# Performance work log

Hardware: AMD Instinct MI355X
Metric: run time of the kernel (lower is better)

The kernel has to match this reference:

```python
import jax, jax.numpy as jnp
import numpy as np

N_HEADS = 16
D_HEAD = 64  # embed_dim // n_heads = 1024 // 16


def setup_inputs() -> dict:
    key = jax.random.key(0)
    ks = jax.random.split(key, 8)
    B, S, E = 2, 2048, 1024
    return {
        "k_in": jax.random.normal(ks[0], (B, S, E), jnp.float32),
        "q_in": jax.random.normal(ks[1], (B, S, E), jnp.float32),
        "v_in": jax.random.normal(ks[2], (B, S, E), jnp.float32),
        "Wq": jax.random.normal(ks[3], (D_HEAD, D_HEAD), jnp.float32) / np.sqrt(D_HEAD),
        "Wk": jax.random.normal(ks[4], (D_HEAD, D_HEAD), jnp.float32) / np.sqrt(D_HEAD),
        "Wv": jax.random.normal(ks[5], (D_HEAD, D_HEAD), jnp.float32) / np.sqrt(D_HEAD),
        "Wo": jax.random.normal(ks[6], (E, E), jnp.float32) / np.sqrt(E),
        "bo": jnp.zeros((E,), jnp.float32),
    }


def reference(k_in, q_in, v_in, Wq, Wk, Wv, Wo, bo):
    B, Sq, E = q_in.shape
    Sk = k_in.shape[1]
    H, Dh = N_HEADS, D_HEAD
    # split heads: [B, S, H, Dh]
    q = q_in.reshape(B, Sq, H, Dh)
    k = k_in.reshape(B, Sk, H, Dh)
    v = v_in.reshape(B, Sk, H, Dh)
    # per-head linear projections (nn.Linear: x @ W.T), then [B, H, S, Dh]
    q = jnp.einsum("bshd,ed->bhse", q, Wq)
    k = jnp.einsum("bshd,ed->bhse", k, Wk)
    v = jnp.einsum("bshd,ed->bhse", v, Wv)
    # scaled dot-product attention
    scores = jnp.einsum("bhqd,bhkd->bhqk", q, k) / jnp.sqrt(jnp.asarray(Dh, q.dtype))
    attn = jax.nn.softmax(scores, axis=-1)
    ctx = jnp.einsum("bhqk,bhkd->bqhd", attn, v)  # [B, Sq, H, Dh]
    concat = ctx.reshape(B, Sq, H * Dh)
    return concat @ Wo.T + bo
```

## Files before the change

### kernel.cpp

```cpp
#include <hip/hip_runtime.h>
#include <hip/hip_fp16.h>

typedef _Float16 f16;
typedef _Float16 f16x8 __attribute__((ext_vector_type(8)));
typedef _Float16 f16x4v __attribute__((ext_vector_type(4)));
typedef float f32x4 __attribute__((ext_vector_type(4)));

#define B_ 2
#define S_ 2048
#define E_ 1024
#define H_ 16
#define DH_ 64

__device__ __forceinline__ f32x4 mfma16(f16x8 a, f16x8 b, f32x4 c) {
    return __builtin_amdgcn_mfma_f32_16x16x32_f16(a, b, c, 0, 0, 0);
}

__device__ __forceinline__ f32x4 vmax4(f32x4 a, f32x4 b) {
    f32x4 r;
    r[0] = fmaxf(a[0], b[0]); r[1] = fmaxf(a[1], b[1]);
    r[2] = fmaxf(a[2], b[2]); r[3] = fmaxf(a[3], b[3]);
    return r;
}

__device__ __forceinline__ f16x8 cvt8(const float* p) {
    float4 v0 = *(const float4*)p;
    float4 v1 = *(const float4*)(p + 4);
    f16x8 r;
    r[0] = (f16)v0.x; r[1] = (f16)v0.y; r[2] = (f16)v0.z; r[3] = (f16)v0.w;
    r[4] = (f16)v1.x; r[5] = (f16)v1.y; r[6] = (f16)v1.z; r[7] = (f16)v1.w;
    return r;
}

__global__ __launch_bounds__(256) void proj_kernel(
    const float* __restrict__ q_in, const float* __restrict__ k_in,
    const float* __restrict__ v_in,
    const float* __restrict__ Wq, const float* __restrict__ Wk,
    const float* __restrict__ Wv,
    f16* __restrict__ Qg, f16* __restrict__ Kg, f16* __restrict__ Vt)
{
    int tid = threadIdx.x;
    int lane = tid & 63, wv = tid >> 6;
    int wid = blockIdx.x * 4 + wv;
    int proj = wid >> 12;
    int r = wid & 4095;
    int bh = r >> 7;
    int stile = r & 127;
    int sbase = stile * 16;
    int h = bh & 15;
    int b = bh >> 4;
    int c = lane & 15, g = lane >> 4;

    const float* x; const float* W;
    if (proj == 0)      { x = q_in; W = Wq; }
    else if (proj == 1) { x = k_in; W = Wk; }
    else                { x = v_in; W = Wv; }

    const float* xrow = x + (((size_t)(b * S_ + sbase + c) * H_ + h) << 6);
    f16x8 a0 = cvt8(xrow + g * 8);
    f16x8 a1 = cvt8(xrow + 32 + g * 8);

    f32x4 acc[4] = {};
#pragma unroll
    for (int nt = 0; nt < 4; ++nt) {
        const float* wrow = W + ((nt * 16 + c) << 6);
        f16x8 b0 = cvt8(wrow + g * 8);
        f16x8 b1 = cvt8(wrow + 32 + g * 8);
        acc[nt] = mfma16(a0, b0, acc[nt]);
        acc[nt] = mfma16(a1, b1, acc[nt]);
    }

    if (proj < 2) {
        f16* out = (proj == 0) ? Qg : Kg;
#pragma unroll
        for (int nt = 0; nt < 4; ++nt)
#pragma unroll
            for (int j = 0; j < 4; ++j) {
                int s = sbase + g * 4 + j;
                out[((size_t)bh * S_ + s) * DH_ + nt * 16 + c] = (f16)acc[nt][j];
            }
    } else {
#pragma unroll
        for (int nt = 0; nt < 4; ++nt) {
            f16x4v pk;
            pk[0] = (f16)acc[nt][0]; pk[1] = (f16)acc[nt][1];
            pk[2] = (f16)acc[nt][2]; pk[3] = (f16)acc[nt][3];
            *(f16x4v*)&Vt[((size_t)bh * DH_ + nt * 16 + c) * S_ + sbase + g * 4] = pk;
        }
    }
}

__global__ __launch_bounds__(256) void cvt_wo(const float* __restrict__ W,
                                              f16* __restrict__ out)
{
    int i = blockIdx.x * 256 + threadIdx.x;
    float4 v = *(const float4*)(W + (size_t)i * 4);
    f16x4v o;
    o[0] = (f16)v.x; o[1] = (f16)v.y; o[2] = (f16)v.z; o[3] = (f16)v.w;
    *(f16x4v*)(out + (size_t)i * 4) = o;
}

#define C1_ 0.18033688011112042f

__global__ __launch_bounds__(512, 4) void attn_kernel(
    const f16* __restrict__ Qg, const f16* __restrict__ Kg,
    const f16* __restrict__ Vt, f16* __restrict__ ctx)
{
    __shared__ __align__(16) f16 Kl[2][128 * 64];
    __shared__ __align__(16) f16 Vl[2][2][64 * 64];
    __shared__ __align__(16) f16 Pl[8][16 * 64];

    int tid = threadIdx.x, lane = tid & 63, wv = tid >> 6;
    int bid = blockIdx.x;
    int sb = (bid & 7) * 64 + (bid >> 3);
    int bh = sb >> 4, qt = sb & 15;
    int b = bh >> 4, h = bh & 15;
    int qbase = qt * 128 + wv * 16;
    int c = lane & 15, g = lane >> 4;
    int swz = (c & 7) << 3;

    const f16* Qh = Qg + (size_t)bh * S_ * DH_;
    const f16* Kh = Kg + (size_t)bh * S_ * DH_;
    const f16* Vh = Vt + (size_t)bh * DH_ * S_;

    int s0 = tid, s1 = tid + 512;
    int kr0 = s0 >> 3, kc0 = s0 & 7, kr1 = s1 >> 3, kc1 = s1 & 7;
    int kd0 = kr0 * 64 + ((kc0 * 8) ^ ((kr0 & 7) << 3));
    int kd1 = kr1 * 64 + ((kc1 * 8) ^ ((kr1 & 7) << 3));
    const f16* ksp0 = Kh + kr0 * 64 + kc0 * 8;
    const f16* ksp1 = Kh + kr1 * 64 + kc1 * 8;
    int vr0 = s0 >> 4, vc0 = s0 & 15, vr1 = s1 >> 4, vc1 = s1 & 15;
    int vst0 = vc0 >> 3, vst1 = vc1 >> 3;
    int vd0 = vr0 * 64 + (((vc0 & 7) * 8) ^ ((vr0 & 7) << 3));
    int vd1 = vr1 * 64 + (((vc1 & 7) * 8) ^ ((vr1 & 7) << 3));
    const f16* vsp0 = Vh + vr0 * S_ + vc0 * 8;
    const f16* vsp1 = Vh + vr1 * S_ + vc1 * 8;

    f16x8 qf[2];
#pragma unroll
    for (int hh = 0; hh < 2; ++hh)
        qf[hh] = *(const f16x8*)(Qh + (size_t)(qbase + c) * DH_ + hh * 32 + g * 8);

    float m2 = -1e30f;
    f32x4 lrv = {};
    f32x4 accO[4] = {};
    f16x8 kreg0, kreg1, vreg0, vreg1;

    kreg0 = *(const f16x8*)ksp0; kreg1 = *(const f16x8*)ksp1;
    vreg0 = *(const f16x8*)vsp0; vreg1 = *(const f16x8*)vsp1;
    *(f16x8*)&Kl[0][kd0] = kreg0; *(f16x8*)&Kl[0][kd1] = kreg1;
    *(f16x8*)&Vl[0][vst0][vd0] = vreg0; *(f16x8*)&Vl[0][vst1][vd1] = vreg1;
    __syncthreads();

#define ATTN_STEP(CUR, T, STAGE)                                               \
    do {                                                                       \
        if (STAGE) {                                                           \
            int ko = ((T) + 1) * 128 * 64, vo = ((T) + 1) * 128;               \
            kreg0 = *(const f16x8*)(ksp0 + ko);                                \
            kreg1 = *(const f16x8*)(ksp1 + ko);                                \
            vreg0 = *(const f16x8*)(vsp0 + vo);                                \
            vreg1 = *(const f16x8*)(vsp1 + vo);                                \
        }                                                                      \
        _Pragma("unroll")                                                      \
        for (int st = 0; st < 2; ++st) {                                       \
            f32x4 accS[4] = {};                                                \
            __builtin_amdgcn_s_setprio(1);                                     \
            _Pragma("unroll")                                                  \
            for (int ks = 0; ks < 4; ++ks) {                                   \
                int krow = (st * 64 + ks * 16 + c) * 64;                       \
                f16x8 k0 = *(const f16x8*)&Kl[CUR][krow + ((8 * g) ^ swz)];    \
                f16x8 k1 = *(const f16x8*)&Kl[CUR][krow + ((32 + 8 * g) ^ swz)];\
                accS[ks] = mfma16(k0, qf[0], accS[ks]);                        \
                accS[ks] = mfma16(k1, qf[1], accS[ks]);                        \
            }                                                                  \
            __builtin_amdgcn_s_setprio(0);                                     \
            f32x4 mx4 = vmax4(vmax4(accS[0], accS[1]), vmax4(accS[2], accS[3]));\
            float rmax = fmaxf(fmaxf(mx4[0], mx4[1]), fmaxf(mx4[2], mx4[3]));  \
            if (!__all(fmaf(rmax, C1_, -m2) <= 8.f)) {                         \
                float mx = fmaxf(rmax, __shfl_xor(rmax, 16));                  \
                mx = fmaxf(mx, __shfl_xor(mx, 32));                            \
                float mn = fmaxf(m2, mx * C1_);                                \
                float al = exp2f(m2 - mn);                                     \
                m2 = mn;                                                       \
                _Pragma("unroll")                                              \
                for (int j = 0; j < 4; ++j) lrv[j] *= al;                      \
                _Pragma("unroll")                                              \
                for (int j = 0; j < 4; ++j) {                                  \
                    float aj = __shfl(al, 4 * g + j);                          \
                    _Pragma("unroll")                                          \
                    for (int nt = 0; nt < 4; ++nt) accO[nt][j] *= aj;          \
                }                                                              \
            }                                                                  \
            _Pragma("unroll")                                                  \
            for (int ks = 0; ks < 4; ++ks) {                                   \
                f32x4 e;                                                       \
                _Pragma("unroll")                                              \
                for (int j = 0; j < 4; ++j)                                    \
                    e[j] = exp2f(fmaf(accS[ks][j], C1_, -m2));                 \
                lrv += e;                                                      \
                f16x4v w;                                                      \
                w[0] = (f16)e[0]; w[1] = (f16)e[1];                            \
                w[2] = (f16)e[2]; w[3] = (f16)e[3];                            \
                *(f16x4v*)&Pl[wv][c * 64 + ((16 * ks + 4 * g) ^ swz)] = w;     \
            }                                                                  \
            __builtin_amdgcn_s_setprio(1);                                     \
            _Pragma("unroll")                                                  \
            for (int kh = 0; kh < 2; ++kh) {                                   \
                f16x8 pa = *(const f16x8*)&Pl[wv][c * 64                       \
                                + (((st * 64 + 32 * kh + 8 * g) & 63) ^ swz)]; \
                _Pragma("unroll")                                              \
                for (int nt = 0; nt < 4; ++nt) {                               \
                    f16x8 vb = *(const f16x8*)&Vl[CUR][st][(nt * 16 + c) * 64  \
                                    + ((32 * kh + 8 * g) ^ swz)];              \
                    accO[nt] = mfma16(pa, vb, accO[nt]);                       \
                }                                                              \
            }                                                                  \
            __builtin_amdgcn_s_setprio(0);                                     \
        }                                                                      \
        if (STAGE) {                                                           \
            int nb = (CUR) ^ 1;                                                \
            *(f16x8*)&Kl[nb][kd0] = kreg0; *(f16x8*)&Kl[nb][kd1] = kreg1;      \
            *(f16x8*)&Vl[nb][vst0][vd0] = vreg0;                               \
            *(f16x8*)&Vl[nb][vst1][vd1] = vreg1;                               \
            __syncthreads();                                                   \
        }                                                                      \
    } while (0)

#pragma unroll 1
    for (int kt = 0; kt < 14; kt += 2) {
        ATTN_STEP(0, kt, 1);
        ATTN_STEP(1, kt + 1, 1);
    }
    ATTN_STEP(0, 14, 1);
    ATTN_STEP(1, 15, 0);
#undef ATTN_STEP

    float lr = (lrv[0] + lrv[1]) + (lrv[2] + lrv[3]);
    lr += __shfl_xor(lr, 16);
    lr += __shfl_xor(lr, 32);
    float inv = 1.f / lr;
#pragma unroll
    for (int j = 0; j < 4; ++j) {
        float lj = __shfl(inv, 4 * g + j);
        int s = qbase + 4 * g + j;
#pragma unroll
        for (int nt = 0; nt < 4; ++nt)
            ctx[((size_t)b * S_ + s) * E_ + h * DH_ + nt * 16 + c] =
                (f16)(accO[nt][j] * lj);
    }
}

__global__ __launch_bounds__(256) void gemm_out(
    const f16* __restrict__ A,
    const f16* __restrict__ Bw,
    const float* __restrict__ bo,
    float* __restrict__ out)
{
    __shared__ __align__(16) f16 Al[2][128 * 64];
    __shared__ __align__(16) f16 Bl[2][64 * 64];

    int tid = threadIdx.x, lane = tid & 63, wv = tid >> 6;
    int bid = blockIdx.x;
    int sb = (bid & 7) * 64 + (bid >> 3);
    int mbase = (sb & 31) * 128, nbase = (sb >> 5) * 64;
    int c = lane & 15, g = lane >> 4;
    int wr = wv >> 1, wc = wv & 1;
    int swz = (c & 7) << 3;

    int adst[4]; const f16* asrc[4];
#pragma unroll
    for (int i = 0; i < 4; ++i) {
        int slot = tid + i * 256;
        int row = slot >> 3, cc = slot & 7;
        adst[i] = row * 64 + ((cc * 8) ^ ((row & 7) << 3));
        asrc[i] = A + (size_t)(mbase + row) * 1024 + cc * 8;
    }
    int bdst[2]; const f16* bsrc[2];
#pragma unroll
    for (int i = 0; i < 2; ++i) {
        int slot = tid + i * 256;
        int row = slot >> 3, cc = slot & 7;
        bdst[i] = row * 64 + ((cc * 8) ^ ((row & 7) << 3));
        bsrc[i] = Bw + (size_t)(nbase + row) * 1024 + cc * 8;
    }

    f32x4 acc[4][2] = {};
    f16x8 areg[4], breg[2];

#pragma unroll
    for (int i = 0; i < 4; ++i) areg[i] = *(const f16x8*)asrc[i];
#pragma unroll
    for (int i = 0; i < 2; ++i) breg[i] = *(const f16x8*)bsrc[i];
#pragma unroll
    for (int i = 0; i < 4; ++i) *(f16x8*)&Al[0][adst[i]] = areg[i];
#pragma unroll
    for (int i = 0; i < 2; ++i) *(f16x8*)&Bl[0][bdst[i]] = breg[i];
    __syncthreads();

#define GEMM_STEP(CUR, T, STAGE)                                               \
    do {                                                                       \
        if (STAGE) {                                                           \
            _Pragma("unroll")                                                  \
            for (int i = 0; i < 4; ++i)                                        \
                areg[i] = *(const f16x8*)(asrc[i] + ((T) + 1) * 64);           \
            _Pragma("unroll")                                                  \
            for (int i = 0; i < 2; ++i)                                        \
                breg[i] = *(const f16x8*)(bsrc[i] + ((T) + 1) * 64);           \
        }                                                                      \
        __builtin_amdgcn_s_setprio(1);                                         \
        _Pragma("unroll")                                                      \
        for (int kk = 0; kk < 2; ++kk) {                                       \
            f16x8 af[4], bf[2];                                                \
            _Pragma("unroll")                                                  \
            for (int mi = 0; mi < 4; ++mi)                                     \
                af[mi] = *(const f16x8*)&Al[CUR][(wr * 64 + mi * 16 + c) * 64  \
                                               + ((32 * kk + 8 * g) ^ swz)];   \
            _Pragma("unroll")                                                  \
            for (int ni = 0; ni < 2; ++ni)                                     \
                bf[ni] = *(const f16x8*)&Bl[CUR][(wc * 32 + ni * 16 + c) * 64  \
                                               + ((32 * kk + 8 * g) ^ swz)];   \
            _Pragma("unroll")                                                  \
            for (int mi = 0; mi < 4; ++mi)                                     \
                _Pragma("unroll")                                              \
                for (int ni = 0; ni < 2; ++ni)                                 \
                    acc[mi][ni] = mfma16(af[mi], bf[ni], acc[mi][ni]);         \
        }                                                                      \
        __builtin_amdgcn_s_setprio(0);                                         \
        if (STAGE) {                                                           \
            int nb = (CUR) ^ 1;                                                \
            _Pragma("unroll")                                                  \
            for (int i = 0; i < 4; ++i) *(f16x8*)&Al[nb][adst[i]] = areg[i];   \
            _Pragma("unroll")                                                  \
            for (int i = 0; i < 2; ++i) *(f16x8*)&Bl[nb][bdst[i]] = breg[i];   \
            __syncthreads();                                                   \
        }                                                                      \
    } while (0)

#pragma unroll 1
    for (int ks = 0; ks < 14; ks += 2) {
        GEMM_STEP(0, ks, 1);
        GEMM_STEP(1, ks + 1, 1);
    }
    GEMM_STEP(0, 14, 1);
    GEMM_STEP(1, 15, 0);
#undef GEMM_STEP

#pragma unroll
    for (int ni = 0; ni < 2; ++ni) {
        float bias = bo[nbase + wc * 32 + ni * 16 + c];
#pragma unroll
        for (int mi = 0; mi < 4; ++mi)
#pragma unroll
            for (int j = 0; j < 4; ++j) {
                int m = mbase + wr * 64 + mi * 16 + g * 4 + j;
                out[(size_t)m * 1024 + nbase + wc * 32 + ni * 16 + c] =
                    acc[mi][ni][j] + bias;
            }
    }
}

extern "C" void kernel_launch(void* const* d_in, const int* in_sizes, int n_in,
                              void* d_out, int out_size, void* d_ws, size_t ws_size,
                              hipStream_t stream)
{
    const float* k_in = (const float*)d_in[0];
    const float* q_in = (const float*)d_in[1];
    const float* v_in = (const float*)d_in[2];
    const float* Wq   = (const float*)d_in[3];
    const float* Wk   = (const float*)d_in[4];
    const float* Wv   = (const float*)d_in[5];
    const float* Wo   = (const float*)d_in[6];
    const float* bo   = (const float*)d_in[7];
    float* out = (float*)d_out;

    char* ws = (char*)d_ws;
    f16* Qg  = (f16*)(ws);
    f16* Kg  = (f16*)(ws + (8u << 20));
    f16* Vt  = (f16*)(ws + (16u << 20));
    f16* ctx = (f16*)(ws + (24u << 20));
    f16* WoH = (f16*)(ws + (32u << 20));

    proj_kernel<<<dim3(3072), dim3(256), 0, stream>>>(q_in, k_in, v_in,
                                                      Wq, Wk, Wv, Qg, Kg, Vt);
    cvt_wo<<<dim3(1024), dim3(256), 0, stream>>>(Wo, WoH);
    attn_kernel<<<dim3(512), dim3(512), 0, stream>>>(Qg, Kg, Vt, ctx);
    gemm_out<<<dim3(512), dim3(256), 0, stream>>>(ctx, WoH, bo, out);
}
```

Before: 115.0 us.

## Shrink attention tiles to 64 keys and 256 threads, fuse Wo conversion into projection

```diff
diff --git a/kernel.cpp b/kernel.cpp
--- a/kernel.cpp
+++ b/kernel.cpp
@@ -2,6 +2,7 @@
 #include <hip/hip_fp16.h>
 
 typedef _Float16 f16;
+typedef __fp16 hf16x2 __attribute__((ext_vector_type(2)));
 typedef _Float16 f16x8 __attribute__((ext_vector_type(8)));
 typedef _Float16 f16x4v __attribute__((ext_vector_type(4)));
 typedef float f32x4 __attribute__((ext_vector_type(4)));
@@ -32,16 +33,27 @@
     return r;
 }
 
-__global__ __launch_bounds__(256) void proj_kernel(
+__global__ __launch_bounds__(256) void proj_cvt_kernel(
     const float* __restrict__ q_in, const float* __restrict__ k_in,
     const float* __restrict__ v_in,
     const float* __restrict__ Wq, const float* __restrict__ Wk,
-    const float* __restrict__ Wv,
-    f16* __restrict__ Qg, f16* __restrict__ Kg, f16* __restrict__ Vt)
+    const float* __restrict__ Wv, const float* __restrict__ Wo,
+    f16* __restrict__ Qg, f16* __restrict__ Kg, f16* __restrict__ Vt,
+    f16* __restrict__ WoH)
 {
     int tid = threadIdx.x;
+    int bx = blockIdx.x;
+    if (bx >= 3072) {
+        int i = (bx - 3072) * 256 + tid;
+        float4 v = *(const float4*)(Wo + (size_t)i * 4);
+        f16x4v o;
+        o[0] = (f16)v.x; o[1] = (f16)v.y; o[2] = (f16)v.z; o[3] = (f16)v.w;
+        *(f16x4v*)(WoH + (size_t)i * 4) = o;
+        return;
+    }
+
     int lane = tid & 63, wv = tid >> 6;
-    int wid = blockIdx.x * 4 + wv;
+    int wid = bx * 4 + wv;
     int proj = wid >> 12;
     int r = wid & 4095;
     int bh = r >> 7;
@@ -90,32 +102,22 @@
     }
 }
 
-__global__ __launch_bounds__(256) void cvt_wo(const float* __restrict__ W,
-                                              f16* __restrict__ out)
-{
-    int i = blockIdx.x * 256 + threadIdx.x;
-    float4 v = *(const float4*)(W + (size_t)i * 4);
-    f16x4v o;
-    o[0] = (f16)v.x; o[1] = (f16)v.y; o[2] = (f16)v.z; o[3] = (f16)v.w;
-    *(f16x4v*)(out + (size_t)i * 4) = o;
-}
-
 #define C1_ 0.18033688011112042f
 
-__global__ __launch_bounds__(512, 4) void attn_kernel(
+__global__ __launch_bounds__(256, 4) void attn_kernel(
     const f16* __restrict__ Qg, const f16* __restrict__ Kg,
     const f16* __restrict__ Vt, f16* __restrict__ ctx)
 {
-    __shared__ __align__(16) f16 Kl[2][128 * 64];
-    __shared__ __align__(16) f16 Vl[2][2][64 * 64];
-    __shared__ __align__(16) f16 Pl[8][16 * 64];
+    __shared__ __align__(16) f16 Kl[2][64 * 64];
+    __shared__ __align__(16) f16 Vl[2][64 * 64];
+    __shared__ __align__(16) f16 Pl[4][16 * 64];
 
     int tid = threadIdx.x, lane = tid & 63, wv = tid >> 6;
     int bid = blockIdx.x;
-    int sb = (bid & 7) * 64 + (bid >> 3);
-    int bh = sb >> 4, qt = sb & 15;
+    int sb = (bid & 7) * 128 + (bid >> 3);
+    int bh = sb >> 5, qt = sb & 31;
     int b = bh >> 4, h = bh & 15;
-    int qbase = qt * 128 + wv * 16;
+    int qbase = qt * 64 + wv * 16;
     int c = lane & 15, g = lane >> 4;
     int swz = (c & 7) << 3;
 
@@ -123,18 +125,14 @@
     const f16* Kh = Kg + (size_t)bh * S_ * DH_;
     const f16* Vh = Vt + (size_t)bh * DH_ * S_;
 
-    int s0 = tid, s1 = tid + 512;
+    int s0 = tid, s1 = tid + 256;
     int kr0 = s0 >> 3, kc0 = s0 & 7, kr1 = s1 >> 3, kc1 = s1 & 7;
     int kd0 = kr0 * 64 + ((kc0 * 8) ^ ((kr0 & 7) << 3));
     int kd1 = kr1 * 64 + ((kc1 * 8) ^ ((kr1 & 7) << 3));
     const f16* ksp0 = Kh + kr0 * 64 + kc0 * 8;
     const f16* ksp1 = Kh + kr1 * 64 + kc1 * 8;
-    int vr0 = s0 >> 4, vc0 = s0 & 15, vr1 = s1 >> 4, vc1 = s1 & 15;
-    int vst0 = vc0 >> 3, vst1 = vc1 >> 3;
-    int vd0 = vr0 * 64 + (((vc0 & 7) * 8) ^ ((vr0 & 7) << 3));
-    int vd1 = vr1 * 64 + (((vc1 & 7) * 8) ^ ((vr1 & 7) << 3));
-    const f16* vsp0 = Vh + vr0 * S_ + vc0 * 8;
-    const f16* vsp1 = Vh + vr1 * S_ + vc1 * 8;
+    const f16* vsp0 = Vh + kr0 * S_ + kc0 * 8;
+    const f16* vsp1 = Vh + kr1 * S_ + kc1 * 8;
 
     f16x8 qf[2];
 #pragma unroll
@@ -149,90 +147,87 @@
     kreg0 = *(const f16x8*)ksp0; kreg1 = *(const f16x8*)ksp1;
     vreg0 = *(const f16x8*)vsp0; vreg1 = *(const f16x8*)vsp1;
     *(f16x8*)&Kl[0][kd0] = kreg0; *(f16x8*)&Kl[0][kd1] = kreg1;
-    *(f16x8*)&Vl[0][vst0][vd0] = vreg0; *(f16x8*)&Vl[0][vst1][vd1] = vreg1;
+    *(f16x8*)&Vl[0][kd0] = vreg0; *(f16x8*)&Vl[0][kd1] = vreg1;
     __syncthreads();
 
 #define ATTN_STEP(CUR, T, STAGE)                                               \
     do {                                                                       \
         if (STAGE) {                                                           \
-            int ko = ((T) + 1) * 128 * 64, vo = ((T) + 1) * 128;               \
+            int ko = ((T) + 1) * 64 * 64, vo = ((T) + 1) * 64;                 \
             kreg0 = *(const f16x8*)(ksp0 + ko);                                \
             kreg1 = *(const f16x8*)(ksp1 + ko);                                \
             vreg0 = *(const f16x8*)(vsp0 + vo);                                \
             vreg1 = *(const f16x8*)(vsp1 + vo);                                \
         }                                                                      \
+        f32x4 accS[4] = {};                                                    \
+        __builtin_amdgcn_s_setprio(1);                                         \
         _Pragma("unroll")                                                      \
-        for (int st = 0; st < 2; ++st) {                                       \
-            f32x4 accS[4] = {};                                                \
-            __builtin_amdgcn_s_setprio(1);                                     \
-            _Pragma("unroll")                                                  \
-            for (int ks = 0; ks < 4; ++ks) {                                   \
-                int krow = (st * 64 + ks * 16 + c) * 64;                       \
-                f16x8 k0 = *(const f16x8*)&Kl[CUR][krow + ((8 * g) ^ swz)];    \
-                f16x8 k1 = *(const f16x8*)&Kl[CUR][krow + ((32 + 8 * g) ^ swz)];\
-                accS[ks] = mfma16(k0, qf[0], accS[ks]);                        \
-                accS[ks] = mfma16(k1, qf[1], accS[ks]);                        \
+        for (int ks = 0; ks < 4; ++ks) {                                       \
+            int krow = (ks * 16 + c) * 64;                                     \
+            f16x8 k0 = *(const f16x8*)&Kl[CUR][krow + ((8 * g) ^ swz)];        \
+            f16x8 k1 = *(const f16x8*)&Kl[CUR][krow + ((32 + 8 * g) ^ swz)];   \
+            accS[ks] = mfma16(k0, qf[0], accS[ks]);                            \
+            accS[ks] = mfma16(k1, qf[1], accS[ks]);                            \
+        }                                                                      \
+        __builtin_amdgcn_s_setprio(0);                                         \
+        f32x4 mx4 = vmax4(vmax4(accS[0], accS[1]), vmax4(accS[2], accS[3]));   \
+        float rmax = fmaxf(fmaxf(mx4[0], mx4[1]), fmaxf(mx4[2], mx4[3]));      \
+        if (!__all(fmaf(rmax, C1_, -m2) <= 8.f)) {                             \
+            float mx = fmaxf(rmax, __shfl_xor(rmax, 16));                      \
+            mx = fmaxf(mx, __shfl_xor(mx, 32));                                \
+            float mn = fmaxf(m2, mx * C1_);                                    \
+            float al = exp2f(m2 - mn);                                         \
+            m2 = mn;                                                           \
+            _Pragma("unroll")                                                  \
+            for (int j = 0; j < 4; ++j) lrv[j] *= al;                          \
+            _Pragma("unroll")                                                  \
+            for (int j = 0; j < 4; ++j) {                                      \
+                float aj = __shfl(al, 4 * g + j);                              \
+                _Pragma("unroll")                                              \
+                for (int nt = 0; nt < 4; ++nt) accO[nt][j] *= aj;              \
             }                                                                  \
-            __builtin_amdgcn_s_setprio(0);                                     \
-            f32x4 mx4 = vmax4(vmax4(accS[0], accS[1]), vmax4(accS[2], accS[3]));\
-            float rmax = fmaxf(fmaxf(mx4[0], mx4[1]), fmaxf(mx4[2], mx4[3]));  \
-            if (!__all(fmaf(rmax, C1_, -m2) <= 8.f)) {                         \
-                float mx = fmaxf(rmax, __shfl_xor(rmax, 16));                  \
-                mx = fmaxf(mx, __shfl_xor(mx, 32));                            \
-                float mn = fmaxf(m2, mx * C1_);                                \
-                float al = exp2f(m2 - mn);                                     \
-                m2 = mn;                                                       \
-                _Pragma("unroll")                                              \
-                for (int j = 0; j < 4; ++j) lrv[j] *= al;                      \
-                _Pragma("unroll")                                              \
-                for (int j = 0; j < 4; ++j) {                                  \
-                    float aj = __shfl(al, 4 * g + j);                          \
-                    _Pragma("unroll")                                          \
-                    for (int nt = 0; nt < 4; ++nt) accO[nt][j] *= aj;          \
-                }                                                              \
+        }                                                                      \
+        _Pragma("unroll")                                                      \
+        for (int ks = 0; ks < 4; ++ks) {                                       \
+            f32x4 e;                                                           \
+            _Pragma("unroll")                                                  \
+            for (int j = 0; j < 4; ++j)                                        \
+                e[j] = exp2f(fmaf(accS[ks][j], C1_, -m2));                     \
+            lrv += e;                                                          \
+            hf16x2 lo = __builtin_amdgcn_cvt_pkrtz(e[0], e[1]);                \
+            hf16x2 hi = __builtin_amdgcn_cvt_pkrtz(e[2], e[3]);                \
+            uint2 w;                                                           \
+            w.x = __builtin_bit_cast(unsigned, lo);                            \
+            w.y = __builtin_bit_cast(unsigned, hi);                            \
+            *(uint2*)&Pl[wv][c * 64 + ((16 * ks + 4 * g) ^ swz)] = w;          \
+        }                                                                      \
+        __builtin_amdgcn_s_setprio(1);                                         \
+        _Pragma("unroll")                                                      \
+        for (int kh = 0; kh < 2; ++kh) {                                       \
+            f16x8 pa = *(const f16x8*)&Pl[wv][c * 64 + ((32 * kh + 8 * g) ^ swz)];\
+            _Pragma("unroll")                                                  \
+            for (int nt = 0; nt < 4; ++nt) {                                   \
+                f16x8 vb = *(const f16x8*)&Vl[CUR][(nt * 16 + c) * 64          \
+                                + ((32 * kh + 8 * g) ^ swz)];                  \
+                accO[nt] = mfma16(pa, vb, accO[nt]);                           \
             }                                                                  \
-            _Pragma("unroll")                                                  \
-            for (int ks = 0; ks < 4; ++ks) {                                   \
-                f32x4 e;                                                       \
-                _Pragma("unroll")                                              \
-                for (int j = 0; j < 4; ++j)                                    \
-                    e[j] = exp2f(fmaf(accS[ks][j], C1_, -m2));                 \
-                lrv += e;                                                      \
-                f16x4v w;                                                      \
-                w[0] = (f16)e[0]; w[1] = (f16)e[1];                            \
-                w[2] = (f16)e[2]; w[3] = (f16)e[3];                            \
-                *(f16x4v*)&Pl[wv][c * 64 + ((16 * ks + 4 * g) ^ swz)] = w;     \
-            }                                                                  \
-            __builtin_amdgcn_s_setprio(1);                                     \
-            _Pragma("unroll")                                                  \
-            for (int kh = 0; kh < 2; ++kh) {                                   \
-                f16x8 pa = *(const f16x8*)&Pl[wv][c * 64                       \
-                                + (((st * 64 + 32 * kh + 8 * g) & 63) ^ swz)]; \
-                _Pragma("unroll")                                              \
-                for (int nt = 0; nt < 4; ++nt) {                               \
-                    f16x8 vb = *(const f16x8*)&Vl[CUR][st][(nt * 16 + c) * 64  \
-                                    + ((32 * kh + 8 * g) ^ swz)];              \
-                    accO[nt] = mfma16(pa, vb, accO[nt]);                       \
-                }                                                              \
-            }                                                                  \
-            __builtin_amdgcn_s_setprio(0);                                     \
-        }                                                                      \
+        }                                                                      \
+        __builtin_amdgcn_s_setprio(0);                                         \
         if (STAGE) {                                                           \
             int nb = (CUR) ^ 1;                                                \
             *(f16x8*)&Kl[nb][kd0] = kreg0; *(f16x8*)&Kl[nb][kd1] = kreg1;      \
-            *(f16x8*)&Vl[nb][vst0][vd0] = vreg0;                               \
-            *(f16x8*)&Vl[nb][vst1][vd1] = vreg1;                               \
+            *(f16x8*)&Vl[nb][kd0] = vreg0; *(f16x8*)&Vl[nb][kd1] = vreg1;      \
             __syncthreads();                                                   \
         }                                                                      \
     } while (0)
 
 #pragma unroll 1
-    for (int kt = 0; kt < 14; kt += 2) {
+    for (int kt = 0; kt < 30; kt += 2) {
         ATTN_STEP(0, kt, 1);
         ATTN_STEP(1, kt + 1, 1);
     }
-    ATTN_STEP(0, 14, 1);
-    ATTN_STEP(1, 15, 0);
+    ATTN_STEP(0, 30, 1);
+    ATTN_STEP(1, 31, 0);
 #undef ATTN_STEP
 
     float lr = (lrv[0] + lrv[1]) + (lrv[2] + lrv[3]);
@@ -380,9 +375,8 @@
     f16* ctx = (f16*)(ws + (24u << 20));
     f16* WoH = (f16*)(ws + (32u << 20));
 
-    proj_kernel<<<dim3(3072), dim3(256), 0, stream>>>(q_in, k_in, v_in,
-                                                      Wq, Wk, Wv, Qg, Kg, Vt);
-    cvt_wo<<<dim3(1024), dim3(256), 0, stream>>>(Wo, WoH);
-    attn_kernel<<<dim3(512), dim3(512), 0, stream>>>(Qg, Kg, Vt, ctx);
+    proj_cvt_kernel<<<dim3(4096), dim3(256), 0, stream>>>(
+        q_in, k_in, v_in, Wq, Wk, Wv, Wo, Qg, Kg, Vt, WoH);
+    attn_kernel<<<dim3(1024), dim3(256), 0, stream>>>(Qg, Kg, Vt, ctx);
     gemm_out<<<dim3(512), dim3(256), 0, stream>>>(ctx, WoH, bo, out);
 }
```

Result: slower. 120.5 us (+4.8%).
